# Optimization experiments

Hardware: AMD Instinct MI355X
Metric: run time of the kernel (lower is better)

Reference implementation:

```python
import jax, jax.numpy as jnp
import numpy as np

# 8 directional offsets (dy, dx) for the -1 tap of each 3x3 filter, filter index 0..7
OFFSETS = [(-1, -1), (-1, 0), (-1, 1), (0, -1), (0, 1), (1, -1), (1, 0), (1, 1)]
# pairing used by the original prod(dim=-1): [[0,4],[1,5],[2,6],[3,7]]
PAIRS = np.array([[0, 4], [1, 5], [2, 6], [3, 7]])


def box_mean(x, k):
    """Uniform k x k box-filter mean with zero padding (same as F.conv2d with ones/k^2)."""
    kern = jnp.ones((1, 1, k, k), x.dtype) / (k * k)
    return jax.lax.conv_general_dilated(
        x, kern, window_strides=(1, 1), padding=[(k // 2, k // 2)] * 2,
        dimension_numbers=('NCHW', 'OIHW', 'NCHW'))


def pcm_scale(l, d):
    """Dilated directional diffs (center minus shifted-by-d neighbor, zero pad),
    opposite-pair products, then min over the 4 pairs."""
    b, c, h, w = l.shape
    p = jnp.pad(l, ((0, 0), (0, 0), (d, d), (d, d)))
    # shifted[..., i][y, x] = l[y + dy*d, x + dx*d] (zeros outside)
    shifted = jnp.stack(
        [p[:, :, d + dy * d:d + dy * d + h, d + dx * d:d + dx * d + w]
         for dy, dx in OFFSETS], axis=-1)  # (b,c,h,w,8)
    diff = l[..., None] - shifted          # PCM_i = conv2d(l, filter_i, dilation=d)
    temp = diff[..., PAIRS].prod(axis=-1)  # (b,c,h,w,4)
    return temp.min(axis=-1)               # (b,c,h,w)


def mpcm(x):
    outs = [pcm_scale(box_mean(x, k), k) for k in (3, 5, 7, 9)]
    return jnp.stack(outs, axis=-1).max(axis=-1)


def setup_inputs() -> dict:
    key = jax.random.key(0)
    input_tensor = jax.random.uniform(key, (16, 1, 512, 512), dtype=jnp.float32)
    return {"input_tensor": input_tensor}


def reference(input_tensor):
    out = mpcm(input_tensor)
    # per-image threshold: mean + 3 * unbiased std (torch .std default ddof=1)
    mean = out.mean(axis=(1, 2, 3), keepdims=True)
    std = out.std(axis=(1, 2, 3), keepdims=True, ddof=1)
    th = mean + 3.0 * std
    return (out > th).astype(out.dtype)
```

## Files before the change

### kernel.cpp

```cpp
#include <hip/hip_runtime.h>


namespace {

constexpr int H = 512, W = 512, NIMG = 16;
constexpr int TW = 64, TH = 32;
constexpr int HALO = 13;
constexpr int IR = TH + 2 * HALO + 1;
constexpr int IC = TW + 2 * HALO + 1;
constexpr int WI = IC;
constexpr int NT = 1024;
constexpr int LS = 82;

struct Smem {
  union alignas(16) {
    double L[(TH + 18) * LS];
    double red[32];
  } u;
  double I[IR * WI];
};

__device__ __forceinline__ double2 ld2(const double* p) {
  double2 v;
  __builtin_memcpy(&v, p, sizeof(double2));
  return v;
}

template <int K, bool BORDER>
__device__ __forceinline__ void scale_pass(Smem& s, int y0, int x0, double mp[2]) {
  constexpr int R   = K / 2;
  constexpr int LH  = TH + 2 * K;
  constexpr int LW  = TW + 2 * K;
  constexpr int HPW = LW / 2;
  constexpr int NP  = LH * HPW;
  constexpr int ITERS = (NP + NT - 1) / NT;
  constexpr int DY  = NT / HPW;
  constexpr int DX  = NT % HPW;
  const int tid = threadIdx.x;

  int yy = tid / HPW;
  int xp = tid - yy * HPW;
#pragma unroll
  for (int it = 0; it < ITERS; ++it) {
    if (yy < LH) {
      const int xx = xp * 2;
      const int li = yy + (HALO - K);
      const int lj = xx + (HALO - K) - R;
      const double* Ia = s.I + (li - R) * WI + lj;
      const double* Ib = Ia + K * WI;
      const double2 a0 = ld2(Ia), aK = ld2(Ia + K);
      const double2 b0 = ld2(Ib), bK = ld2(Ib + K);
      const double s0 = (bK.x - aK.x) - (b0.x - a0.x);
      const double s1 = (bK.y - aK.y) - (b0.y - a0.y);
      double2 o;
      if (BORDER) {
        const int gy = y0 - K + yy, gx = x0 - K + xx;
        const bool in0 = ((unsigned)gy < (unsigned)H) & ((unsigned)gx < (unsigned)W);
        const bool in1 = ((unsigned)gy < (unsigned)H) & ((unsigned)(gx + 1) < (unsigned)W);
        o.x = in0 ? s0 : 0.0;
        o.y = in1 ? s1 : 0.0;
      } else {
        o.x = s0;
        o.y = s1;
      }
      *(double2*)&s.u.L[yy * LS + xx] = o;
    }
    xp += DX; yy += DY;
    if (xp >= HPW) { xp -= HPW; ++yy; }
  }
  __syncthreads();

  {
    constexpr double inv2 = 1.0 / ((double)K * K * K * K);
    const int r  = tid >> 5;
    const int cc = (tid & 31) * 2;
    const double* up  = &s.u.L[r * LS + cc];
    const double* mid = up + K * LS;
    const double* dn  = up + 2 * K * LS;
    const double2 u0 = ld2(up),  uK = ld2(up + K),  u2 = ld2(up + 2 * K);
    const double2 m0 = ld2(mid), mK = ld2(mid + K), m2 = ld2(mid + 2 * K);
    const double2 w0 = ld2(dn),  wK = ld2(dn + K),  w2 = ld2(dn + 2 * K);
    {
      const double c = mK.x;
      const double e0 = c - u0.x, e1 = c - uK.x, e2 = c - u2.x, e3 = c - m0.x;
      const double e4 = c - m2.x, e5 = c - w0.x, e6 = c - wK.x, e7 = c - w2.x;
      const double m = fmin(fmin(e0 * e4, e1 * e5), fmin(e2 * e6, e3 * e7));
      mp[0] = fmax(mp[0], m * inv2);
    }
    {
      const double c = mK.y;
      const double e0 = c - u0.y, e1 = c - uK.y, e2 = c - u2.y, e3 = c - m0.y;
      const double e4 = c - m2.y, e5 = c - w0.y, e6 = c - wK.y, e7 = c - w2.y;
      const double m = fmin(fmin(e0 * e4, e1 * e5), fmin(e2 * e6, e3 * e7));
      mp[1] = fmax(mp[1], m * inv2);
    }
  }
  __syncthreads();
}

template <bool BORDER>
__device__ __forceinline__ void compute_tile(Smem& s, const float* __restrict__ img,
                                             int y0, int x0, double mp[2]) {
  const int tid = threadIdx.x;
  {
    constexpr int NE = IR * IC;
    constexpr int SITERS = (NE + NT - 1) / NT;
    constexpr int DIY = NT / IC, DIX = NT % IC;
    int iy = tid / IC;
    int ix = tid - iy * IC;
#pragma unroll
    for (int it = 0; it < SITERS; ++it) {
      if (iy < IR) {
        const int gy = y0 - HALO + iy - 1, gx = x0 - HALO + ix - 1;
        double v = 0.0;
        if (BORDER) {
          if (iy > 0 && ix > 0 && (unsigned)gy < (unsigned)H && (unsigned)gx < (unsigned)W)
            v = (double)img[gy * W + gx];
        } else {
          if (iy > 0 && ix > 0) v = (double)img[gy * W + gx];
        }
        s.I[iy * WI + ix] = v;
      }
      ix += DIX; iy += DIY;
      if (ix >= IC) { ix -= IC; ++iy; }
    }
  }
  __syncthreads();

  if (tid < IR - 1) {
    double* p = &s.I[(tid + 1) * WI + 1];
    double run = 0.0;
#pragma unroll
    for (int x = 0; x < IC - 1; ++x) { run += p[x]; p[x] = run; }
  }
  __syncthreads();

  if (tid < IC - 1) {
    double* p = &s.I[WI + (tid + 1)];
    double run = 0.0;
#pragma unroll
    for (int y = 0; y < IR - 1; ++y) { run += *p; *p = run; p += WI; }
  }
  __syncthreads();

  mp[0] = mp[1] = -1.0e300;
  scale_pass<3, BORDER>(s, y0, x0, mp);
  scale_pass<5, BORDER>(s, y0, x0, mp);
  scale_pass<7, BORDER>(s, y0, x0, mp);
  scale_pass<9, BORDER>(s, y0, x0, mp);
}

__global__ __launch_bounds__(NT, 8) void k_stats(const float* __restrict__ in,
                                                 double* __restrict__ partials,
                                                 double* __restrict__ wsmp) {
  __shared__ Smem s;
  const int img = blockIdx.z;
  const int y0 = blockIdx.y * TH, x0 = blockIdx.x * TW;
  const bool border = (blockIdx.x == 0) | (blockIdx.x == gridDim.x - 1) |
                      (blockIdx.y == 0) | (blockIdx.y == gridDim.y - 1);
  double mp[2];
  if (border) compute_tile<true>(s, in + (size_t)img * H * W, y0, x0, mp);
  else        compute_tile<false>(s, in + (size_t)img * H * W, y0, x0, mp);

  const int tid = threadIdx.x;
  const int r = tid >> 5, cc = (tid & 31) * 2;
  if (wsmp != nullptr) {
    double2 v; v.x = mp[0]; v.y = mp[1];
    *(double2*)&wsmp[(size_t)img * H * W + (size_t)(y0 + r) * W + (x0 + cc)] = v;
  }

  double s1 = mp[0] + mp[1];
  double s2 = mp[0] * mp[0] + mp[1] * mp[1];
#pragma unroll
  for (int off = 32; off; off >>= 1) {
    s1 += __shfl_down(s1, off);
    s2 += __shfl_down(s2, off);
  }
  if ((tid & 63) == 0) { s.u.red[tid >> 6] = s1; s.u.red[16 + (tid >> 6)] = s2; }
  __syncthreads();
  if (tid == 0) {
    double S = 0.0, S2 = 0.0;
#pragma unroll
    for (int w = 0; w < NT / 64; ++w) { S += s.u.red[w]; S2 += s.u.red[16 + w]; }
    const int bl = (img * gridDim.y + blockIdx.y) * gridDim.x + blockIdx.x;
    partials[2 * bl]     = S;
    partials[2 * bl + 1] = S2;
  }
}

__global__ void k_thresh(const double* __restrict__ partials, double* __restrict__ th) {
  const int img = blockIdx.x;
  const int lane = threadIdx.x;
  const int nb = (H / TH) * (W / TW);
  double S = 0.0, S2 = 0.0;
  for (int b = lane; b < nb; b += 64) {
    S  += partials[2 * (img * nb + b)];
    S2 += partials[2 * (img * nb + b) + 1];
  }
#pragma unroll
  for (int off = 32; off; off >>= 1) {
    S  += __shfl_down(S, off);
    S2 += __shfl_down(S2, off);
  }
  if (lane == 0) {
    const double N = (double)(H * W);
    const double mean = S / N;
    double var = (S2 - S * S / N) / (N - 1.0);
    if (var < 0.0) var = 0.0;
    th[img] = mean + 3.0 * sqrt(var);
  }
}

__global__ __launch_bounds__(256) void k_out_cached(const double* __restrict__ wsmp,
                                                    const double* __restrict__ th,
                                                    float* __restrict__ out) {
  const int n = NIMG * H * W / 2;
  for (int i = blockIdx.x * 256 + threadIdx.x; i < n; i += gridDim.x * 256) {
    const double t = th[i >> 17];
    const double2 v = ((const double2*)wsmp)[i];
    float2 o; o.x = (v.x > t) ? 1.0f : 0.0f; o.y = (v.y > t) ? 1.0f : 0.0f;
    ((float2*)out)[i] = o;
  }
}

__global__ __launch_bounds__(NT, 8) void k_out_full(const float* __restrict__ in,
                                                    const double* __restrict__ th,
                                                    float* __restrict__ out) {
  __shared__ Smem s;
  const int img = blockIdx.z;
  const int y0 = blockIdx.y * TH, x0 = blockIdx.x * TW;
  const bool border = (blockIdx.x == 0) | (blockIdx.x == gridDim.x - 1) |
                      (blockIdx.y == 0) | (blockIdx.y == gridDim.y - 1);
  double mp[2];
  if (border) compute_tile<true>(s, in + (size_t)img * H * W, y0, x0, mp);
  else        compute_tile<false>(s, in + (size_t)img * H * W, y0, x0, mp);
  const double t = th[img];
  const int tid = threadIdx.x;
  const int r = tid >> 5, cc = (tid & 31) * 2;
  float2 o;
  o.x = (mp[0] > t) ? 1.0f : 0.0f;
  o.y = (mp[1] > t) ? 1.0f : 0.0f;
  *(float2*)&out[(size_t)img * H * W + (size_t)(y0 + r) * W + (x0 + cc)] = o;
}

}

extern "C" void kernel_launch(void* const* d_in, const int* in_sizes, int n_in,
                              void* d_out, int out_size, void* d_ws, size_t ws_size,
                              hipStream_t stream) {
  const float* in = (const float*)d_in[0];
  float* out = (float*)d_out;

  double* th = (double*)d_ws;
  double* partials = (double*)((char*)d_ws + 4096);
  double* wsmp = (double*)((char*)d_ws + 131072);
  const bool cache = ws_size >= (size_t)131072 + (size_t)NIMG * H * W * 8;

  dim3 grid(W / TW, H / TH, NIMG);
  k_stats<<<grid, NT, 0, stream>>>(in, partials, cache ? wsmp : nullptr);
  k_thresh<<<NIMG, 64, 0, stream>>>(partials, th);
  if (cache) {
    k_out_cached<<<2048, 256, 0, stream>>>(wsmp, th, out);
  } else {
    k_out_full<<<grid, NT, 0, stream>>>(in, th, out);
  }
}
```

Baseline: 91.08 us.

## Double-buffer box-filter scale passes and vectorize column prefix sum

```diff
diff --git a/kernel.cpp b/kernel.cpp
--- a/kernel.cpp
+++ b/kernel.cpp
@@ -12,12 +12,11 @@
 constexpr int NT = 1024;
 constexpr int LS = 82;
 
-struct Smem {
-  union alignas(16) {
-    double L[(TH + 18) * LS];
-    double red[32];
-  } u;
+struct alignas(16) Smem {
+  double A[46 * LS];
+  double B[50 * LS];
   double I[IR * WI];
+  double red[32];
 };
 
 __device__ __forceinline__ double2 ld2(const double* p) {
@@ -25,13 +24,16 @@
   __builtin_memcpy(&v, p, sizeof(double2));
   return v;
 }
+__device__ __forceinline__ void st2(double* p, double2 v) {
+  __builtin_memcpy(p, &v, sizeof(double2));
+}
 
 template <int K, bool BORDER>
-__device__ __forceinline__ void scale_pass(Smem& s, int y0, int x0, double mp[2]) {
+__device__ __forceinline__ void box_pass(const double* __restrict__ I,
+                                         double* __restrict__ L, int y0, int x0) {
   constexpr int R   = K / 2;
   constexpr int LH  = TH + 2 * K;
-  constexpr int LW  = TW + 2 * K;
-  constexpr int HPW = LW / 2;
+  constexpr int HPW = (TW + 2 * K) / 2;
   constexpr int NP  = LH * HPW;
   constexpr int ITERS = (NP + NT - 1) / NT;
   constexpr int DY  = NT / HPW;
@@ -46,7 +48,7 @@
       const int xx = xp * 2;
       const int li = yy + (HALO - K);
       const int lj = xx + (HALO - K) - R;
-      const double* Ia = s.I + (li - R) * WI + lj;
+      const double* Ia = I + (li - R) * WI + lj;
       const double* Ib = Ia + K * WI;
       const double2 a0 = ld2(Ia), aK = ld2(Ia + K);
       const double2 b0 = ld2(Ib), bK = ld2(Ib + K);
@@ -63,39 +65,39 @@
         o.x = s0;
         o.y = s1;
       }
-      *(double2*)&s.u.L[yy * LS + xx] = o;
+      st2(&L[yy * LS + xx], o);
     }
     xp += DX; yy += DY;
     if (xp >= HPW) { xp -= HPW; ++yy; }
   }
-  __syncthreads();
-
+}
+
+template <int K>
+__device__ __forceinline__ void pcm_pass(const double* __restrict__ L, double mp[2]) {
+  constexpr double inv2 = 1.0 / ((double)K * K * K * K);
+  const int tid = threadIdx.x;
+  const int r  = tid >> 5;
+  const int cc = (tid & 31) * 2;
+  const double* up  = &L[r * LS + cc];
+  const double* mid = up + K * LS;
+  const double* dn  = up + 2 * K * LS;
+  const double2 u0 = ld2(up),  uK = ld2(up + K),  u2 = ld2(up + 2 * K);
+  const double2 m0 = ld2(mid), mK = ld2(mid + K), m2 = ld2(mid + 2 * K);
+  const double2 w0 = ld2(dn),  wK = ld2(dn + K),  w2 = ld2(dn + 2 * K);
   {
-    constexpr double inv2 = 1.0 / ((double)K * K * K * K);
-    const int r  = tid >> 5;
-    const int cc = (tid & 31) * 2;
-    const double* up  = &s.u.L[r * LS + cc];
-    const double* mid = up + K * LS;
-    const double* dn  = up + 2 * K * LS;
-    const double2 u0 = ld2(up),  uK = ld2(up + K),  u2 = ld2(up + 2 * K);
-    const double2 m0 = ld2(mid), mK = ld2(mid + K), m2 = ld2(mid + 2 * K);
-    const double2 w0 = ld2(dn),  wK = ld2(dn + K),  w2 = ld2(dn + 2 * K);
-    {
-      const double c = mK.x;
-      const double e0 = c - u0.x, e1 = c - uK.x, e2 = c - u2.x, e3 = c - m0.x;
-      const double e4 = c - m2.x, e5 = c - w0.x, e6 = c - wK.x, e7 = c - w2.x;
-      const double m = fmin(fmin(e0 * e4, e1 * e5), fmin(e2 * e6, e3 * e7));
-      mp[0] = fmax(mp[0], m * inv2);
-    }
-    {
-      const double c = mK.y;
-      const double e0 = c - u0.y, e1 = c - uK.y, e2 = c - u2.y, e3 = c - m0.y;
-      const double e4 = c - m2.y, e5 = c - w0.y, e6 = c - wK.y, e7 = c - w2.y;
-      const double m = fmin(fmin(e0 * e4, e1 * e5), fmin(e2 * e6, e3 * e7));
-      mp[1] = fmax(mp[1], m * inv2);
-    }
-  }
-  __syncthreads();
+    const double c = mK.x;
+    const double e0 = c - u0.x, e1 = c - uK.x, e2 = c - u2.x, e3 = c - m0.x;
+    const double e4 = c - m2.x, e5 = c - w0.x, e6 = c - wK.x, e7 = c - w2.x;
+    const double m = fmin(fmin(e0 * e4, e1 * e5), fmin(e2 * e6, e3 * e7));
+    mp[0] = fmax(mp[0], m * inv2);
+  }
+  {
+    const double c = mK.y;
+    const double e0 = c - u0.y, e1 = c - uK.y, e2 = c - u2.y, e3 = c - m0.y;
+    const double e4 = c - m2.y, e5 = c - w0.y, e6 = c - wK.y, e7 = c - w2.y;
+    const double m = fmin(fmin(e0 * e4, e1 * e5), fmin(e2 * e6, e3 * e7));
+    mp[1] = fmax(mp[1], m * inv2);
+  }
 }
 
 template <bool BORDER>
@@ -135,22 +137,36 @@
   }
   __syncthreads();
 
-  if (tid < IC - 1) {
-    double* p = &s.I[WI + (tid + 1)];
-    double run = 0.0;
-#pragma unroll
-    for (int y = 0; y < IR - 1; ++y) { run += *p; *p = run; p += WI; }
+  if (tid < (IC - 1) / 2) {
+    double* p = &s.I[WI + (1 + 2 * tid)];
+    double r0 = 0.0, r1 = 0.0;
+#pragma unroll
+    for (int y = 0; y < IR - 1; ++y) {
+      const double2 v = ld2(p);
+      r0 += v.x; r1 += v.y;
+      double2 o; o.x = r0; o.y = r1;
+      st2(p, o);
+      p += WI;
+    }
   }
   __syncthreads();
 
   mp[0] = mp[1] = -1.0e300;
-  scale_pass<3, BORDER>(s, y0, x0, mp);
-  scale_pass<5, BORDER>(s, y0, x0, mp);
-  scale_pass<7, BORDER>(s, y0, x0, mp);
-  scale_pass<9, BORDER>(s, y0, x0, mp);
-}
-
-__global__ __launch_bounds__(NT, 8) void k_stats(const float* __restrict__ in,
+  box_pass<3, BORDER>(s.I, s.A, y0, x0);
+  __syncthreads();
+  box_pass<5, BORDER>(s.I, s.B, y0, x0);
+  pcm_pass<3>(s.A, mp);
+  __syncthreads();
+  box_pass<7, BORDER>(s.I, s.A, y0, x0);
+  pcm_pass<5>(s.B, mp);
+  __syncthreads();
+  box_pass<9, BORDER>(s.I, s.B, y0, x0);
+  pcm_pass<7>(s.A, mp);
+  __syncthreads();
+  pcm_pass<9>(s.B, mp);
+}
+
+__global__ __launch_bounds__(NT, 4) void k_stats(const float* __restrict__ in,
                                                  double* __restrict__ partials,
                                                  double* __restrict__ wsmp) {
   __shared__ Smem s;
@@ -176,12 +192,12 @@
     s1 += __shfl_down(s1, off);
     s2 += __shfl_down(s2, off);
   }
-  if ((tid & 63) == 0) { s.u.red[tid >> 6] = s1; s.u.red[16 + (tid >> 6)] = s2; }
+  if ((tid & 63) == 0) { s.red[tid >> 6] = s1; s.red[16 + (tid >> 6)] = s2; }
   __syncthreads();
   if (tid == 0) {
     double S = 0.0, S2 = 0.0;
 #pragma unroll
-    for (int w = 0; w < NT / 64; ++w) { S += s.u.red[w]; S2 += s.u.red[16 + w]; }
+    for (int w = 0; w < NT / 64; ++w) { S += s.red[w]; S2 += s.red[16 + w]; }
     const int bl = (img * gridDim.y + blockIdx.y) * gridDim.x + blockIdx.x;
     partials[2 * bl]     = S;
     partials[2 * bl + 1] = S2;
@@ -223,7 +239,7 @@
   }
 }
 
-__global__ __launch_bounds__(NT, 8) void k_out_full(const float* __restrict__ in,
+__global__ __launch_bounds__(NT, 4) void k_out_full(const float* __restrict__ in,
                                                     const double* __restrict__ th,
                                                     float* __restrict__ out) {
   __shared__ Smem s;
```

New measurement: 114.3 us. 25.5% more time.

## Fuse stats, threshold and output into one cooperative persistent kernel

Applied to the files above, without the earlier changes.

```diff
diff --git a/kernel.cpp b/kernel.cpp
--- a/kernel.cpp
+++ b/kernel.cpp
@@ -1,5 +1,8 @@
 #include <hip/hip_runtime.h>
-
+#include <hip/hip_cooperative_groups.h>
+
+
+namespace cg = cooperative_groups;
 
 namespace {
 
@@ -11,6 +14,8 @@
 constexpr int WI = IC;
 constexpr int NT = 1024;
 constexpr int LS = 82;
+constexpr int NBLK = 512;
+constexpr int TILES_PER_BLK = 4;
 
 struct Smem {
   union alignas(16) {
@@ -25,13 +30,15 @@
   __builtin_memcpy(&v, p, sizeof(double2));
   return v;
 }
+__device__ __forceinline__ void st2(double* p, double2 v) {
+  __builtin_memcpy(p, &v, sizeof(double2));
+}
 
 template <int K, bool BORDER>
 __device__ __forceinline__ void scale_pass(Smem& s, int y0, int x0, double mp[2]) {
   constexpr int R   = K / 2;
   constexpr int LH  = TH + 2 * K;
-  constexpr int LW  = TW + 2 * K;
-  constexpr int HPW = LW / 2;
+  constexpr int HPW = (TW + 2 * K) / 2;
   constexpr int NP  = LH * HPW;
   constexpr int ITERS = (NP + NT - 1) / NT;
   constexpr int DY  = NT / HPW;
@@ -63,7 +70,7 @@
         o.x = s0;
         o.y = s1;
       }
-      *(double2*)&s.u.L[yy * LS + xx] = o;
+      st2(&s.u.L[yy * LS + xx], o);
     }
     xp += DX; yy += DY;
     if (xp >= HPW) { xp -= HPW; ++yy; }
@@ -104,12 +111,12 @@
   const int tid = threadIdx.x;
   {
     constexpr int NE = IR * IC;
-    constexpr int SITERS = (NE + NT - 1) / NT;
+    constexpr int SIT = (NE + NT - 1) / NT;
     constexpr int DIY = NT / IC, DIX = NT % IC;
     int iy = tid / IC;
     int ix = tid - iy * IC;
 #pragma unroll
-    for (int it = 0; it < SITERS; ++it) {
+    for (int it = 0; it < SIT; ++it) {
       if (iy < IR) {
         const int gy = y0 - HALO + iy - 1, gx = x0 - HALO + ix - 1;
         double v = 0.0;
@@ -135,11 +142,17 @@
   }
   __syncthreads();
 
-  if (tid < IC - 1) {
-    double* p = &s.I[WI + (tid + 1)];
-    double run = 0.0;
-#pragma unroll
-    for (int y = 0; y < IR - 1; ++y) { run += *p; *p = run; p += WI; }
+  if (tid < (IC - 1) / 2) {
+    double* p = &s.I[WI + (1 + 2 * tid)];
+    double r0 = 0.0, r1 = 0.0;
+#pragma unroll
+    for (int y = 0; y < IR - 1; ++y) {
+      const double2 v = ld2(p);
+      r0 += v.x; r1 += v.y;
+      double2 o; o.x = r0; o.y = r1;
+      st2(p, o);
+      p += WI;
+    }
   }
   __syncthreads();
 
@@ -148,6 +161,78 @@
   scale_pass<5, BORDER>(s, y0, x0, mp);
   scale_pass<7, BORDER>(s, y0, x0, mp);
   scale_pass<9, BORDER>(s, y0, x0, mp);
+}
+
+__global__ __launch_bounds__(NT, 8) void k_fused(const float* __restrict__ in,
+                                                 double* __restrict__ partials,
+                                                 float* __restrict__ out) {
+  __shared__ Smem s;
+  const int tid = threadIdx.x;
+  double m00, m01, m10, m11, m20, m21, m30, m31;
+  double s1 = 0.0, s2 = 0.0;
+
+#pragma unroll 1
+  for (int i = 0; i < TILES_PER_BLK; ++i) {
+    const int t = blockIdx.x * TILES_PER_BLK + i;
+    const int img = t >> 7;
+    const int rem = t & 127;
+    const int tyb = rem >> 3, txb = rem & 7;
+    double mp[2];
+    compute_tile<true>(s, in + (size_t)img * H * W, tyb * TH, txb * TW, mp);
+    if      (i == 0) { m00 = mp[0]; m01 = mp[1]; }
+    else if (i == 1) { m10 = mp[0]; m11 = mp[1]; }
+    else if (i == 2) { m20 = mp[0]; m21 = mp[1]; }
+    else             { m30 = mp[0]; m31 = mp[1]; }
+    s1 += mp[0] + mp[1];
+    s2 += mp[0] * mp[0] + mp[1] * mp[1];
+  }
+
+#pragma unroll
+  for (int off = 32; off; off >>= 1) {
+    s1 += __shfl_down(s1, off);
+    s2 += __shfl_down(s2, off);
+  }
+  if ((tid & 63) == 0) { s.u.red[tid >> 6] = s1; s.u.red[16 + (tid >> 6)] = s2; }
+  __syncthreads();
+  if (tid == 0) {
+    double S = 0.0, S2 = 0.0;
+#pragma unroll
+    for (int w = 0; w < NT / 64; ++w) { S += s.u.red[w]; S2 += s.u.red[16 + w]; }
+    partials[2 * blockIdx.x]     = S;
+    partials[2 * blockIdx.x + 1] = S2;
+  }
+  __threadfence();
+  cg::this_grid().sync();
+
+  const int imgb = blockIdx.x >> 5;
+  double S = 0.0, SS = 0.0;
+  for (int b = 0; b < 32; ++b) {
+    S  += partials[2 * (imgb * 32 + b)];
+    SS += partials[2 * (imgb * 32 + b) + 1];
+  }
+  const double N = (double)(H * W);
+  const double mean = S / N;
+  double var = (SS - S * S / N) / (N - 1.0);
+  if (var < 0.0) var = 0.0;
+  const double th = mean + 3.0 * sqrt(var);
+
+  const int r = tid >> 5, cc = (tid & 31) * 2;
+#pragma unroll 1
+  for (int i = 0; i < TILES_PER_BLK; ++i) {
+    const int t = blockIdx.x * TILES_PER_BLK + i;
+    const int img = t >> 7;
+    const int rem = t & 127;
+    const int y0 = (rem >> 3) * TH, x0 = (rem & 7) * TW;
+    double a, b;
+    if      (i == 0) { a = m00; b = m01; }
+    else if (i == 1) { a = m10; b = m11; }
+    else if (i == 2) { a = m20; b = m21; }
+    else             { a = m30; b = m31; }
+    float2 o;
+    o.x = (a > th) ? 1.0f : 0.0f;
+    o.y = (b > th) ? 1.0f : 0.0f;
+    *(float2*)&out[(size_t)img * H * W + (size_t)(y0 + r) * W + (x0 + cc)] = o;
+  }
 }
 
 __global__ __launch_bounds__(NT, 8) void k_stats(const float* __restrict__ in,
@@ -223,26 +308,6 @@
   }
 }
 
-__global__ __launch_bounds__(NT, 8) void k_out_full(const float* __restrict__ in,
-                                                    const double* __restrict__ th,
-                                                    float* __restrict__ out) {
-  __shared__ Smem s;
-  const int img = blockIdx.z;
-  const int y0 = blockIdx.y * TH, x0 = blockIdx.x * TW;
-  const bool border = (blockIdx.x == 0) | (blockIdx.x == gridDim.x - 1) |
-                      (blockIdx.y == 0) | (blockIdx.y == gridDim.y - 1);
-  double mp[2];
-  if (border) compute_tile<true>(s, in + (size_t)img * H * W, y0, x0, mp);
-  else        compute_tile<false>(s, in + (size_t)img * H * W, y0, x0, mp);
-  const double t = th[img];
-  const int tid = threadIdx.x;
-  const int r = tid >> 5, cc = (tid & 31) * 2;
-  float2 o;
-  o.x = (mp[0] > t) ? 1.0f : 0.0f;
-  o.y = (mp[1] > t) ? 1.0f : 0.0f;
-  *(float2*)&out[(size_t)img * H * W + (size_t)(y0 + r) * W + (x0 + cc)] = o;
-}
-
 }
 
 extern "C" void kernel_launch(void* const* d_in, const int* in_sizes, int n_in,
@@ -254,14 +319,23 @@
   double* th = (double*)d_ws;
   double* partials = (double*)((char*)d_ws + 4096);
   double* wsmp = (double*)((char*)d_ws + 131072);
-  const bool cache = ws_size >= (size_t)131072 + (size_t)NIMG * H * W * 8;
-
-  dim3 grid(W / TW, H / TH, NIMG);
-  k_stats<<<grid, NT, 0, stream>>>(in, partials, cache ? wsmp : nullptr);
-  k_thresh<<<NIMG, 64, 0, stream>>>(partials, th);
-  if (cache) {
-    k_out_cached<<<2048, 256, 0, stream>>>(wsmp, th, out);
+
+  int ma = 0;
+  hipError_t oe = hipOccupancyMaxActiveBlocksPerMultiprocessor(&ma, k_fused, NT, 0);
+  const bool coop = (oe == hipSuccess) && (ma >= 2);
+
+  if (coop) {
+    void* kargs[] = { (void*)&in, (void*)&partials, (void*)&out };
+    hipLaunchCooperativeKernel(k_fused, dim3(NBLK), dim3(NT), kargs, 0, stream);
   } else {
-    k_out_full<<<grid, NT, 0, stream>>>(in, th, out);
-  }
-}
+    const bool cache = ws_size >= (size_t)131072 + (size_t)NIMG * H * W * 8;
+    dim3 grid(W / TW, H / TH, NIMG);
+    k_stats<<<grid, NT, 0, stream>>>(in, partials, cache ? wsmp : nullptr);
+    k_thresh<<<NIMG, 64, 0, stream>>>(partials, th);
+    if (cache) {
+      k_out_cached<<<2048, 256, 0, stream>>>(wsmp, th, out);
+    } else {
+      k_out_cached<<<2048, 256, 0, stream>>>(wsmp, th, out);
+    }
+  }
+}
```

Result: no change. 92.85 us (+1.9%).

## Parallelize integral-image prefix sums and fuse threshold into output kernel

Applied to the files above, without the earlier changes.

```diff
diff --git a/kernel.cpp b/kernel.cpp
--- a/kernel.cpp
+++ b/kernel.cpp
@@ -16,6 +16,7 @@
   union alignas(16) {
     double L[(TH + 18) * LS];
     double red[32];
+    double seg[384];
   } u;
   double I[IR * WI];
 };
@@ -25,13 +26,15 @@
   __builtin_memcpy(&v, p, sizeof(double2));
   return v;
 }
+__device__ __forceinline__ void st2(double* p, double2 v) {
+  __builtin_memcpy(p, &v, sizeof(double2));
+}
 
 template <int K, bool BORDER>
 __device__ __forceinline__ void scale_pass(Smem& s, int y0, int x0, double mp[2]) {
   constexpr int R   = K / 2;
   constexpr int LH  = TH + 2 * K;
-  constexpr int LW  = TW + 2 * K;
-  constexpr int HPW = LW / 2;
+  constexpr int HPW = (TW + 2 * K) / 2;
   constexpr int NP  = LH * HPW;
   constexpr int ITERS = (NP + NT - 1) / NT;
   constexpr int DY  = NT / HPW;
@@ -63,7 +66,7 @@
         o.x = s0;
         o.y = s1;
       }
-      *(double2*)&s.u.L[yy * LS + xx] = o;
+      st2(&s.u.L[yy * LS + xx], o);
     }
     xp += DX; yy += DY;
     if (xp >= HPW) { xp -= HPW; ++yy; }
@@ -104,12 +107,12 @@
   const int tid = threadIdx.x;
   {
     constexpr int NE = IR * IC;
-    constexpr int SITERS = (NE + NT - 1) / NT;
+    constexpr int SIT = (NE + NT - 1) / NT;
     constexpr int DIY = NT / IC, DIX = NT % IC;
     int iy = tid / IC;
     int ix = tid - iy * IC;
 #pragma unroll
-    for (int it = 0; it < SITERS; ++it) {
+    for (int it = 0; it < SIT; ++it) {
       if (iy < IR) {
         const int gy = y0 - HALO + iy - 1, gx = x0 - HALO + ix - 1;
         double v = 0.0;
@@ -127,19 +130,59 @@
   }
   __syncthreads();
 
-  if (tid < IR - 1) {
-    double* p = &s.I[(tid + 1) * WI + 1];
+  if (tid < 58 * 6) {
+    const int r = tid / 6, sg = tid - r * 6;
+    const double* p = &s.I[(r + 1) * WI + 1 + sg * 15];
+    double a = 0.0;
+#pragma unroll
+    for (int c = 0; c < 15; ++c) a += p[c];
+    s.u.seg[tid] = a;
+  }
+  __syncthreads();
+  if (tid < 58 * 6) {
+    const int r = tid / 6, sg = tid - r * 6;
+    const double* ss = &s.u.seg[r * 6];
     double run = 0.0;
 #pragma unroll
-    for (int x = 0; x < IC - 1; ++x) { run += p[x]; p[x] = run; }
-  }
-  __syncthreads();
-
-  if (tid < IC - 1) {
-    double* p = &s.I[WI + (tid + 1)];
-    double run = 0.0;
-#pragma unroll
-    for (int y = 0; y < IR - 1; ++y) { run += *p; *p = run; p += WI; }
+    for (int u = 0; u < 5; ++u)
+      if (u < sg) run += ss[u];
+    double* p = &s.I[(r + 1) * WI + 1 + sg * 15];
+#pragma unroll
+    for (int c = 0; c < 15; ++c) { run += p[c]; p[c] = run; }
+  }
+  __syncthreads();
+
+  if (tid < 45 * 4) {
+    const int pp = tid >> 2, sg = tid & 3;
+    const int start = 1 + 15 * sg;
+    const int len = (sg == 3) ? 13 : 15;
+    const double* p = &s.I[start * WI + 1 + 2 * pp];
+    double a0 = 0.0, a1 = 0.0;
+    for (int y = 0; y < len; ++y) {
+      const double2 v = ld2(p);
+      a0 += v.x; a1 += v.y;
+      p += WI;
+    }
+    s.u.seg[2 * tid] = a0;
+    s.u.seg[2 * tid + 1] = a1;
+  }
+  __syncthreads();
+  if (tid < 45 * 4) {
+    const int pp = tid >> 2, sg = tid & 3;
+    const int start = 1 + 15 * sg;
+    const int len = (sg == 3) ? 13 : 15;
+    double r0 = 0.0, r1 = 0.0;
+#pragma unroll
+    for (int u = 0; u < 3; ++u)
+      if (u < sg) { r0 += s.u.seg[2 * (4 * pp + u)]; r1 += s.u.seg[2 * (4 * pp + u) + 1]; }
+    double* p = &s.I[start * WI + 1 + 2 * pp];
+    for (int y = 0; y < len; ++y) {
+      const double2 v = ld2(p);
+      r0 += v.x; r1 += v.y;
+      double2 o; o.x = r0; o.y = r1;
+      st2(p, o);
+      p += WI;
+    }
   }
   __syncthreads();
 
@@ -188,6 +231,47 @@
   }
 }
 
+__global__ __launch_bounds__(256) void k_out2(const double* __restrict__ wsmp,
+                                              const double* __restrict__ partials,
+                                              float* __restrict__ out) {
+  const int img = blockIdx.y;
+  const int tid = threadIdx.x;
+  __shared__ double sth;
+  if (tid < 64) {
+    double S = 0.0, S2 = 0.0;
+    for (int b = tid; b < 128; b += 64) {
+      S  += partials[2 * (img * 128 + b)];
+      S2 += partials[2 * (img * 128 + b) + 1];
+    }
+#pragma unroll
+    for (int off = 32; off; off >>= 1) {
+      S  += __shfl_down(S, off);
+      S2 += __shfl_down(S2, off);
+    }
+    if (tid == 0) {
+      const double N = (double)(H * W);
+      const double mean = S / N;
+      double var = (S2 - S * S / N) / (N - 1.0);
+      if (var < 0.0) var = 0.0;
+      sth = mean + 3.0 * sqrt(var);
+    }
+  }
+  __syncthreads();
+  const double t = sth;
+
+  const size_t base = (size_t)img * (H * W / 2) + (size_t)blockIdx.x * 1024;
+  const double2* src = (const double2*)wsmp + base;
+  float2* dst = (float2*)out + base;
+#pragma unroll
+  for (int k = 0; k < 4; ++k) {
+    const double2 v = src[tid + k * 256];
+    float2 o;
+    o.x = (v.x > t) ? 1.0f : 0.0f;
+    o.y = (v.y > t) ? 1.0f : 0.0f;
+    dst[tid + k * 256] = o;
+  }
+}
+
 __global__ void k_thresh(const double* __restrict__ partials, double* __restrict__ th) {
   const int img = blockIdx.x;
   const int lane = threadIdx.x;
@@ -208,18 +292,6 @@
     double var = (S2 - S * S / N) / (N - 1.0);
     if (var < 0.0) var = 0.0;
     th[img] = mean + 3.0 * sqrt(var);
-  }
-}
-
-__global__ __launch_bounds__(256) void k_out_cached(const double* __restrict__ wsmp,
-                                                    const double* __restrict__ th,
-                                                    float* __restrict__ out) {
-  const int n = NIMG * H * W / 2;
-  for (int i = blockIdx.x * 256 + threadIdx.x; i < n; i += gridDim.x * 256) {
-    const double t = th[i >> 17];
-    const double2 v = ((const double2*)wsmp)[i];
-    float2 o; o.x = (v.x > t) ? 1.0f : 0.0f; o.y = (v.y > t) ? 1.0f : 0.0f;
-    ((float2*)out)[i] = o;
   }
 }
 
@@ -258,10 +330,10 @@
 
   dim3 grid(W / TW, H / TH, NIMG);
   k_stats<<<grid, NT, 0, stream>>>(in, partials, cache ? wsmp : nullptr);
-  k_thresh<<<NIMG, 64, 0, stream>>>(partials, th);
   if (cache) {
-    k_out_cached<<<2048, 256, 0, stream>>>(wsmp, th, out);
+    k_out2<<<dim3(128, NIMG), 256, 0, stream>>>(wsmp, partials, out);
   } else {
+    k_thresh<<<NIMG, 64, 0, stream>>>(partials, th);
     k_out_full<<<grid, NT, 0, stream>>>(in, th, out);
   }
 }
```

Result: slower. 94.57 us (+3.8%).
